# Kernel tuning notes

Measured on AMD Instinct MI355X. Metric: run time of the kernel, lower is better.

The kernel has to match this reference:

```python
import jax, jax.numpy as jnp
import numpy as np

LAT = 4; K = 4; NP = 3 * K - 1; HID = 16; NT = 10; BOUND = 5.0
_in_deg = np.arange(1, LAT + 1)
_hd = (np.arange(HID) % (LAT - 1)) + 1
M1 = jnp.asarray((_hd[:, None] >= _in_deg[None, :]).astype(np.float32))  # [HID, LAT]
M2 = jnp.asarray((_hd[:, None] >= _hd[None, :]).astype(np.float32))      # [HID, HID]
M3 = jnp.asarray((np.repeat(_in_deg, NP)[:, None] > _hd[None, :]).astype(np.float32))  # [LAT*NP, HID]


def _subm(x, m, w, b):
    # submanifold conv: inactive inputs are zero, output restricted to active sites
    y = jax.lax.conv_general_dilated(x, w, (1, 1), 'SAME', dimension_numbers=('NHWC', 'HWIO', 'NHWC')) + b
    return jnp.where(m[..., None], y, 0.0)


def _maxpool(x, m, kh, kw):
    neg = jnp.asarray(-1e30, x.dtype)
    xm = jnp.where(m[..., None], x, neg)
    y = jax.lax.reduce_window(xm, neg, jax.lax.max, (1, kh, kw, 1), (1, kh, kw, 1), 'VALID')
    mo = jax.lax.reduce_window(m.astype(x.dtype), 0.0, jax.lax.max, (1, kh, kw), (1, kh, kw), 'VALID') > 0
    return jnp.where(mo[..., None], y, 0.0), mo


def _invconv(x, w, b, mo):
    # sparse inverse conv with kernel == stride of paired pool: non-overlapping transposed conv
    kh, kw, ci, co = w.shape
    B, h, wd, _ = x.shape
    y = jnp.einsum('bhwc,ijcd->bhiwjd', x, w).reshape(B, h * kh, wd * kw, co) + b
    return jnp.where(mo[..., None], y, 0.0)


def _rqs(x, uw, uh, ud):
    # monotonic rational-quadratic spline, identity outside [-BOUND, BOUND]
    shp = x.shape
    widths = jax.nn.softmax(uw, -1) * (2 * BOUND)
    heights = jax.nn.softmax(uh, -1) * (2 * BOUND)
    edge = jnp.full(shp + (1,), -BOUND, x.dtype)
    xk = jnp.concatenate([edge, jnp.cumsum(widths, -1) - BOUND], -1)
    yk = jnp.concatenate([edge, jnp.cumsum(heights, -1) - BOUND], -1)
    one = jnp.ones(shp + (1,), x.dtype)
    dk = jnp.concatenate([one, jax.nn.softplus(ud), one], -1)
    inside = (x >= -BOUND) & (x <= BOUND)
    xc = jnp.clip(x, -BOUND, BOUND)
    idx = jnp.clip(jnp.sum((xc[..., None] >= xk[..., :-1]).astype(jnp.int32), -1) - 1, 0, K - 1)[..., None]
    g = lambda a, i: jnp.take_along_axis(a, i, -1)[..., 0]
    x0, x1 = g(xk, idx), g(xk, idx + 1)
    y0, y1 = g(yk, idx), g(yk, idx + 1)
    d0, d1 = g(dk, idx), g(dk, idx + 1)
    dx = x1 - x0
    dy = y1 - y0
    s = dy / dx
    t = (xc - x0) / dx
    den = s + (d1 + d0 - 2 * s) * t * (1 - t)
    y = y0 + dy * (s * t * t + d0 * t * (1 - t)) / den
    ld = jnp.log(s * s * (d1 * t * t + 2 * s * t * (1 - t) + d0 * (1 - t) ** 2)) - 2 * jnp.log(den)
    return jnp.where(inside, y, x), jnp.where(inside, ld, 0.0)


def _nsf(z, fW1, fb1, fW2, fb2, fW3, fb3):
    ld_tot = jnp.zeros(z.shape[:-1], z.dtype)
    for t in range(NT):
        h = jax.nn.relu(z @ (fW1[t] * M1).T + fb1[t])
        h = jax.nn.relu(h @ (fW2[t] * M2).T + fb2[t])
        p = (h @ (fW3[t] * M3).T + fb3[t]).reshape(z.shape[:-1] + (LAT, NP))
        z, ld = _rqs(z, p[..., :K], p[..., K:2 * K], p[..., 2 * K:])
        ld_tot = ld_tot + ld.sum(-1)
        if t < NT - 1:
            z = z[..., ::-1]
    return z, ld_tot


def _forward(x, eps, w1, b1, w2, b2, w3, b3, wmu, bmu, wlv, blv, wlin, blin, u1, bu1, w4, b4, u2, bu2, w5, b5, u3, bu3, w6, b6, fW1, fb1, fW2, fb2, fW3, fb3):
    xn = jnp.transpose(x, (0, 2, 3, 1))  # NCHW -> NHWC
    m0 = jnp.any(xn != 0, axis=-1)       # active sites (spconv from_dense)
    lrelu = lambda v: jax.nn.leaky_relu(v, 0.01)
    y = lrelu(_subm(xn, m0, w1, b1))
    y, m1 = _maxpool(y, m0, 2, 2)
    y = lrelu(_subm(y, m1, w2, b2))
    y, m2 = _maxpool(y, m1, 5, 2)
    y = lrelu(_subm(y, m2, w3, b3))
    y, m3 = _maxpool(y, m2, 5, 2)        # [B, 4, 16, 32]
    mu = jnp.where(m3[..., None], y @ wmu.T + bmu, 0.0)
    logvar = jnp.where(m3[..., None], y @ wlv.T + blv, 0.0)
    std = jnp.exp(0.5 * logvar)
    z0 = mu + eps * std
    z, log_det = _nsf(z0, fW1, fb1, fW2, fb2, fW3, fb3)
    LOG2PI = 1.8378770664093453
    log_q0 = jnp.sum(-0.5 * ((z0 - mu) / std) ** 2 - jnp.log(std) - 0.5 * LOG2PI, -1)
    log_p = jnp.sum(-0.5 * z * z - 0.5 * LOG2PI, -1)
    kld_pc = log_q0 - log_det - log_p
    kld = jnp.sum(jnp.where(m3, kld_pc, 0.0), axis=(1, 2))  # index_add over batch indices
    zf = jnp.where(m3[..., None], z, 0.0)
    dec = jnp.where(m3[..., None], zf @ wlin.T + blin, 0.0)
    y = _invconv(dec, u1, bu1, m2)
    y = _subm(y, m2, w4, b4)
    y = _invconv(y, u2, bu2, m1)
    y = _subm(y, m1, w5, b5)
    y = _invconv(y, u3, bu3, m0)
    y = _subm(y, m0, w6, b6)
    out = jnp.transpose(y, (0, 3, 1, 2))  # back to NCHW like .dense()
    return out, mu, logvar, kld, zf


def setup_inputs():
    key = jax.random.key(0)
    ks = iter(jax.random.split(key, 80))
    B, C, H, W = 128, 6, 200, 128
    d = {}
    x = jax.random.normal(next(ks), (B, C, H, W), jnp.float32)
    keep = jax.random.uniform(next(ks), (B, 1, H, W)) < 0.15
    d['x'] = jnp.where(keep, x, 0.0)
    d['eps'] = jax.random.normal(next(ks), (B, 4, 16, LAT), jnp.float32)
    def p(name, shape, s=0.1):
        d[name] = jax.random.normal(next(ks), shape, jnp.float32) * s
    p('w1', (3, 3, 6, 8)); p('b1', (8,))
    p('w2', (3, 3, 8, 16)); p('b2', (16,))
    p('w3', (3, 3, 16, 32)); p('b3', (32,))
    p('wmu', (LAT, 32)); p('bmu', (LAT,))
    p('wlv', (LAT, 32)); p('blv', (LAT,))
    p('wlin', (32, LAT)); p('blin', (32,))
    p('u1', (5, 2, 32, 32)); p('bu1', (32,))
    p('w4', (3, 3, 32, 16)); p('b4', (16,))
    p('u2', (5, 2, 16, 16)); p('bu2', (16,))
    p('w5', (3, 3, 16, 8)); p('b5', (8,))
    p('u3', (2, 2, 8, 8)); p('bu3', (8,))
    p('w6', (3, 3, 8, 6)); p('b6', (6,))
    p('fW1', (NT, HID, LAT)); p('fb1', (NT, HID))
    p('fW2', (NT, HID, HID)); p('fb2', (NT, HID))
    p('fW3', (NT, LAT * NP, HID)); p('fb3', (NT, LAT * NP))
    return d


def reference(x, eps, w1, b1, w2, b2, w3, b3, wmu, bmu, wlv, blv, wlin, blin, u1, bu1, w4, b4, u2, bu2, w5, b5, u3, bu3, w6, b6, fW1, fb1, fW2, fb2, fW3, fb3):
    return _forward(x, eps, w1, b1, w2, b2, w3, b3, wmu, bmu, wlv, blv, wlin, blin, u1, bu1, w4, b4, u2, bu2, w5, b5, u3, bu3, w6, b6, fW1, fb1, fW2, fb2, fW3, fb3)
```

## Files before the change

### kernel.cpp

```cpp
#include <hip/hip_runtime.h>
#include <math.h>

constexpr int NB=128;
constexpr int NH0=200, NW0=128, NC0=6;
constexpr int NH1=100, NW1=64,  NC1=8;
constexpr int NH2=20,  NW2=32,  NC2=16;
constexpr int NH3=4,   NW3=16,  NC3=32;
constexpr int LAT=4, NPp=11, HID=16, NT=10;
constexpr float BOUNDf=5.0f;
constexpr float LOG2PI=1.8378770664093453f;

__device__ __forceinline__ float fexpf(float v){ return __expf(v); }
__device__ __forceinline__ float flogf(float v){ return __logf(v); }
__device__ __forceinline__ float softplusf(float v){ return v>20.f ? v : __logf(1.f+__expf(v)); }
__device__ __forceinline__ float lrelu(float v){ return v>0.f ? v : 0.01f*v; }

__global__ __launch_bounds__(256) void k_conv1pool(
    const float* __restrict__ x, const float* __restrict__ w1, const float* __restrict__ b1,
    float* __restrict__ y1p, unsigned char* __restrict__ m0, unsigned char* __restrict__ m1){
  __shared__ float xs[6][18][24];
  __shared__ float ws1[54][8];
  __shared__ float b1s[8];
  int blk = blockIdx.x;
  int b  = blk / 104;
  int t  = blk % 104;
  int th = t >> 3, tw = t & 7;
  int h0 = th*16, w0 = tw*16;
  int tid = threadIdx.x;
  for (int i=tid;i<432;i+=256) ws1[i>>3][i&7] = w1[i];
  if (tid<8) b1s[tid]=b1[tid];
  for (int i=tid;i<6*18*18;i+=256){
    int ci=i/324; int rem=i-ci*324; int r=rem/18, c=rem-r*18;
    int h=h0-1+r, w=w0-1+c;
    float v=0.f;
    if (h>=0 && h<NH0 && w>=0 && w<NW0) v = x[((size_t)(b*NC0+ci)*NH0+h)*NW0+w];
    xs[ci][r][c]=v;
  }
  __syncthreads();
  int r = tid>>4, c = tid&15;
  int h = h0+r, w = w0+c;
  bool inb = (h < NH0);
  float c0v=xs[0][r+1][c+1], c1v=xs[1][r+1][c+1], c2v=xs[2][r+1][c+1];
  float c3v=xs[3][r+1][c+1], c4v=xs[4][r+1][c+1], c5v=xs[5][r+1][c+1];
  bool act = inb && ((c0v!=0.f)||(c1v!=0.f)||(c2v!=0.f)||(c3v!=0.f)||(c4v!=0.f)||(c5v!=0.f));
  if (inb) m0[(b*NH0+h)*NW0+w] = act?1:0;
  float a[8];
  #pragma unroll
  for (int co=0;co<8;co++) a[co]=b1s[co];
  #pragma unroll 1
  for (int kh=0;kh<3;kh++)
  #pragma unroll 1
  for (int kw=0;kw<3;kw++){
    #pragma unroll
    for (int ci=0;ci<6;ci++){
      float v = xs[ci][r+kh][c+kw];
      const float* wv = ws1[(kh*3+kw)*6+ci];
      #pragma unroll
      for (int co=0;co<8;co++) a[co]=fmaf(v,wv[co],a[co]);
    }
  }
  #pragma unroll
  for (int co=0;co<8;co++) a[co] = act ? lrelu(a[co]) : -1e30f;
  float best[8];
  #pragma unroll
  for (int co=0;co<8;co++){
    float v = a[co];
    v = fmaxf(v, __shfl_xor(v,1));
    v = fmaxf(v, __shfl_xor(v,16));
    best[co]=v;
  }
  float af = act?1.f:0.f;
  af = fmaxf(af, __shfl_xor(af,1));
  af = fmaxf(af, __shfl_xor(af,16));
  bool anyact = af>0.f;
  bool rep = ((r&1)==0) && ((c&1)==0);
  if (rep && inb){
    int hp=h>>1, wp=w>>1;
    float4 o0,o1;
    if (anyact){
      o0=make_float4(best[0],best[1],best[2],best[3]);
      o1=make_float4(best[4],best[5],best[6],best[7]);
    } else { o0=make_float4(0,0,0,0); o1=o0; }
    float4* yp = (float4*)(y1p + (((size_t)b*NH1+hp)*NW1+wp)*8);
    yp[0]=o0; yp[1]=o1;
    m1[(b*NH1+hp)*NW1+wp] = anyact?1:0;
  }
}

__global__ __launch_bounds__(256) void k_conv2pool(
    const float* __restrict__ yin, const unsigned char* __restrict__ m1,
    const float* __restrict__ w2, const float* __restrict__ b2,
    float* __restrict__ yout, unsigned char* __restrict__ m2){
  __shared__ float ys[8][27][35];
  __shared__ unsigned char msl[27][35];
  __shared__ float w2s[72][16];
  __shared__ float b2s[16];
  int blk = blockIdx.x;
  int b  = blk >> 3;
  int t  = blk & 7;
  int th = t >> 1, tw = t & 1;
  int r0 = th*25 - 1, c0 = tw*32 - 1;
  int tid = threadIdx.x;
  for (int i=tid;i<1152;i+=256) w2s[i>>4][i&15] = w2[i];
  if (tid<16) b2s[tid]=b2[tid];
  for (int p=tid;p<27*34;p+=256){
    int r=p/34, c=p-(p/34)*34;
    int h1=r0+r, w1c=c0+c;
    bool ok = (h1>=0 && h1<NH1 && w1c>=0 && w1c<NW1);
    msl[r][c] = ok ? m1[(b*NH1+h1)*NW1+w1c] : 0;
    float4 v0=make_float4(0,0,0,0), v1=v0;
    if (ok){
      const float4* pp = (const float4*)(yin + (((size_t)b*NH1+h1)*NW1+w1c)*8);
      v0=pp[0]; v1=pp[1];
    }
    ys[0][r][c]=v0.x; ys[1][r][c]=v0.y; ys[2][r][c]=v0.z; ys[3][r][c]=v0.w;
    ys[4][r][c]=v1.x; ys[5][r][c]=v1.y; ys[6][r][c]=v1.z; ys[7][r][c]=v1.w;
  }
  __syncthreads();
  if (tid < 160){
    int oid = tid >> 1, coq = tid & 1;
    int co0 = coq*8;
    int lh = oid >> 4, lw = oid & 15;
    int h2 = th*5+lh, w2c = tw*16+lw;
    float best[8];
    #pragma unroll
    for (int co=0;co<8;co++) best[co]=-1e30f;
    bool many=false;
    #pragma unroll 1
    for (int i=0;i<5;i++)
    #pragma unroll 1
    for (int j=0;j<2;j++){
      int r = lh*5+i+1, c = lw*2+j+1;
      if (!msl[r][c]) continue;
      many=true;
      float a[8];
      #pragma unroll
      for (int co=0;co<8;co++) a[co]=b2s[co0+co];
      #pragma unroll 1
      for (int kh=0;kh<3;kh++)
      #pragma unroll 1
      for (int kw=0;kw<3;kw++){
        #pragma unroll
        for (int ci=0;ci<8;ci++){
          float v = ys[ci][r-1+kh][c-1+kw];
          const float* wr = w2s[(kh*3+kw)*8+ci];
          #pragma unroll
          for (int co=0;co<8;co++) a[co]=fmaf(v,wr[co0+co],a[co]);
        }
      }
      #pragma unroll
      for (int co=0;co<8;co++) best[co]=fmaxf(best[co], lrelu(a[co]));
    }
    float4 o0,o1;
    if (many){
      o0=make_float4(best[0],best[1],best[2],best[3]);
      o1=make_float4(best[4],best[5],best[6],best[7]);
    } else { o0=make_float4(0,0,0,0); o1=o0; }
    float4* op = (float4*)(yout + (((size_t)b*NH2+h2)*NW2+w2c)*16 + co0);
    op[0]=o0; op[1]=o1;
    if (coq==0) m2[(b*NH2+h2)*NW2+w2c] = many?1:0;
  }
}

__global__ __launch_bounds__(256) void k_conv3pool(
    const float* __restrict__ yin, const unsigned char* __restrict__ m2,
    const float* __restrict__ w3, const float* __restrict__ b3,
    float* __restrict__ yout, unsigned char* __restrict__ m3,
    float* __restrict__ out_kld){
  __shared__ float ys[16][20][33];
  __shared__ unsigned char msl[20][32];
  __shared__ float w3s[144][32];
  __shared__ float b3s[32];
  int b = blockIdx.x;
  int tid = threadIdx.x;
  if (tid==0) out_kld[b]=0.f;
  for (int i=tid;i<4608;i+=256) w3s[i>>5][i&31] = w3[i];
  if (tid<32) b3s[tid]=b3[tid];
  for (int p=tid;p<640;p+=256){
    int r=p>>5, c=p&31;
    msl[r][c] = m2[(b*NH2+r)*NW2+c];
    const float4* pp = (const float4*)(yin + (((size_t)b*NH2+r)*NW2+c)*16);
    float4 q0=pp[0],q1=pp[1],q2=pp[2],q3=pp[3];
    ys[0][r][c]=q0.x; ys[1][r][c]=q0.y; ys[2][r][c]=q0.z; ys[3][r][c]=q0.w;
    ys[4][r][c]=q1.x; ys[5][r][c]=q1.y; ys[6][r][c]=q1.z; ys[7][r][c]=q1.w;
    ys[8][r][c]=q2.x; ys[9][r][c]=q2.y; ys[10][r][c]=q2.z; ys[11][r][c]=q2.w;
    ys[12][r][c]=q3.x; ys[13][r][c]=q3.y; ys[14][r][c]=q3.z; ys[15][r][c]=q3.w;
  }
  __syncthreads();
  int p = tid>>2, coq = tid&3;
  int co0 = coq*8;
  int hp = p>>4, wp = p&15;
  float best[8];
  #pragma unroll
  for (int co=0;co<8;co++) best[co]=-1e30f;
  bool many=false;
  #pragma unroll 1
  for (int i=0;i<5;i++)
  #pragma unroll 1
  for (int j=0;j<2;j++){
    int h2 = hp*5+i, w2c = wp*2+j;
    if (!msl[h2][w2c]) continue;
    many=true;
    float a[8];
    #pragma unroll
    for (int co=0;co<8;co++) a[co]=b3s[co0+co];
    #pragma unroll 1
    for (int kh=0;kh<3;kh++){
      int hh=h2+kh-1;
      if (hh<0||hh>=NH2) continue;
      #pragma unroll 1
      for (int kw=0;kw<3;kw++){
        int ww=w2c+kw-1;
        if (ww<0||ww>=NW2) continue;
        #pragma unroll
        for (int ci=0;ci<16;ci++){
          float v = ys[ci][hh][ww];
          const float* wr = w3s[(kh*3+kw)*16+ci];
          #pragma unroll
          for (int co=0;co<8;co++) a[co]=fmaf(v,wr[co0+co],a[co]);
        }
      }
    }
    #pragma unroll
    for (int co=0;co<8;co++) best[co]=fmaxf(best[co], lrelu(a[co]));
  }
  float4 o0,o1;
  if (many){
    o0=make_float4(best[0],best[1],best[2],best[3]);
    o1=make_float4(best[4],best[5],best[6],best[7]);
  } else { o0=make_float4(0,0,0,0); o1=o0; }
  float4* op = (float4*)(yout + ((size_t)(b*64+p))*32 + co0);
  op[0]=o0; op[1]=o1;
  if (coq==0) m3[b*64+p] = many?1:0;
}

__global__ __launch_bounds__(64) void k_latent(
    const float* __restrict__ y3p, const unsigned char* __restrict__ m3,
    const float* __restrict__ eps,
    const float* __restrict__ wmu, const float* __restrict__ bmu,
    const float* __restrict__ wlv, const float* __restrict__ blv,
    const float* __restrict__ wlin, const float* __restrict__ blin,
    const float* __restrict__ fW1, const float* __restrict__ fb1,
    const float* __restrict__ fW2, const float* __restrict__ fb2,
    const float* __restrict__ fW3, const float* __restrict__ fb3,
    float* __restrict__ out_mu, float* __restrict__ out_lv,
    float* __restrict__ out_kld, float* __restrict__ out_zf,
    float* __restrict__ dec)
{
  __shared__ __align__(16) float sW1[NT*HID*LAT];
  __shared__ float sb1[NT*HID];
  __shared__ __align__(16) float sW2[NT*HID*HID];
  __shared__ float sb2[NT*HID];
  __shared__ __align__(16) float sW3[NT*LAT*NPp*HID];
  __shared__ float sb3[NT*LAT*NPp];
  __shared__ __align__(16) float swmu[LAT*NC3];
  __shared__ __align__(16) float swlv[LAT*NC3];
  __shared__ __align__(16) float slin[NC3*LAT];
  __shared__ float sbmu[LAT], sblv[LAT], sblin[NC3];
  int tid = threadIdx.x;
  for (int i=tid;i<NT*HID*LAT;i+=64){ int j=i&3; int r=(i>>2)%HID; sW1[i]=fW1[i]*(((r%3+1)>=(j+1))?1.f:0.f); }
  for (int i=tid;i<NT*HID;i+=64){ sb1[i]=fb1[i]; sb2[i]=fb2[i]; }
  for (int i=tid;i<NT*HID*HID;i+=64){ int j=i&15; int r=(i>>4)%HID; sW2[i]=fW2[i]*(((r%3+1)>=(j%3+1))?1.f:0.f); }
  for (int i=tid;i<NT*LAT*NPp*HID;i+=64){ int j=i&15; int r=(i>>4)%(LAT*NPp); sW3[i]=fW3[i]*(((r/NPp+1)>(j%3+1))?1.f:0.f); }
  for (int i=tid;i<NT*LAT*NPp;i+=64) sb3[i]=fb3[i];
  for (int i=tid;i<LAT*NC3;i+=64){ swmu[i]=wmu[i]; swlv[i]=wlv[i]; slin[i]=wlin[i]; }
  if (tid<LAT){ sbmu[tid]=bmu[tid]; sblv[tid]=blv[tid]; }
  for (int i=tid;i<NC3;i+=64) sblin[i]=blin[i];
  __syncthreads();

  int blk = blockIdx.x;
  int b   = blk >> 2;
  int gpos = b*64 + (blk&3)*16 + (tid>>2);
  int g = tid & 3;
  bool msk = m3[gpos]!=0;
  float kld_part = 0.f;
  if (msk){
    const float4* yp = (const float4*)(y3p + (size_t)gpos*NC3);
    const float4* wm = (const float4*)(swmu + g*NC3);
    const float4* wl = (const float4*)(swlv + g*NC3);
    float mu_g = sbmu[g], lv_g = sblv[g];
    #pragma unroll
    for (int q=0;q<8;q++){
      float4 yq = yp[q], a = wm[q], c = wl[q];
      mu_g = fmaf(yq.x,a.x, fmaf(yq.y,a.y, fmaf(yq.z,a.z, fmaf(yq.w,a.w, mu_g))));
      lv_g = fmaf(yq.x,c.x, fmaf(yq.y,c.y, fmaf(yq.z,c.z, fmaf(yq.w,c.w, lv_g))));
    }
    float std_g = fexpf(0.5f*lv_g);
    float ev_g  = eps[(size_t)gpos*LAT+g];
    float z0_g  = fmaf(ev_g, std_g, mu_g);
    float zg = z0_g;
    float z[4];
    z[g]=zg; z[g^1]=__shfl_xor(zg,1); z[g^2]=__shfl_xor(zg,2); z[g^3]=__shfl_xor(zg,3);
    float ld_g = 0.f;
    for (int t=0;t<NT;t++){
      float h1[16];
      const float4* W1t = (const float4*)(sW1 + t*HID*LAT);
      const float*  b1t = sb1 + t*HID;
      #pragma unroll
      for (int i2=0;i2<16;i2++){
        float4 w = W1t[i2];
        float a = b1t[i2];
        a = fmaf(z[0],w.x, fmaf(z[1],w.y, fmaf(z[2],w.z, fmaf(z[3],w.w, a))));
        h1[i2]=fmaxf(a,0.f);
      }
      float h2o[4];
      const float* W2t = sW2 + t*HID*HID;
      const float* b2t = sb2 + t*HID;
      #pragma unroll
      for (int k=0;k<4;k++){
        int row = g*4+k;
        const float4* wr = (const float4*)(W2t + row*HID);
        float a = b2t[row];
        #pragma unroll
        for (int q=0;q<4;q++){
          float4 w = wr[q];
          a = fmaf(h1[q*4+0],w.x, fmaf(h1[q*4+1],w.y, fmaf(h1[q*4+2],w.z, fmaf(h1[q*4+3],w.w, a))));
        }
        h2o[k]=fmaxf(a,0.f);
      }
      float h2[16];
      #pragma unroll
      for (int k=0;k<4;k++) h2[g*4+k]=h2o[k];
      #pragma unroll
      for (int mski=1;mski<4;mski++){
        int og = g^mski;
        #pragma unroll
        for (int k=0;k<4;k++) h2[og*4+k]=__shfl_xor(h2o[k],mski);
      }
      float p[NPp];
      const float* W3t = sW3 + t*LAT*NPp*HID;
      const float* b3t = sb3 + t*LAT*NPp;
      #pragma unroll
      for (int r=0;r<NPp;r++){
        int row = g*NPp+r;
        const float4* wr = (const float4*)(W3t + row*HID);
        float a = b3t[row];
        #pragma unroll
        for (int q=0;q<4;q++){
          float4 w = wr[q];
          a = fmaf(h2[q*4+0],w.x, fmaf(h2[q*4+1],w.y, fmaf(h2[q*4+2],w.z, fmaf(h2[q*4+3],w.w, a))));
        }
        p[r]=a;
      }
      float mw=fmaxf(fmaxf(p[0],p[1]),fmaxf(p[2],p[3]));
      float e0=fexpf(p[0]-mw), e1=fexpf(p[1]-mw), e2=fexpf(p[2]-mw), e3=fexpf(p[3]-mw);
      float wsc=10.f/(e0+e1+e2+e3);
      float xk1=fmaf(e0,wsc,-BOUNDf), xk2=fmaf(e1,wsc,xk1), xk3=fmaf(e2,wsc,xk2), xk4=fmaf(e3,wsc,xk3);
      float mh=fmaxf(fmaxf(p[4],p[5]),fmaxf(p[6],p[7]));
      float f0=fexpf(p[4]-mh), f1=fexpf(p[5]-mh), f2=fexpf(p[6]-mh), f3=fexpf(p[7]-mh);
      float hsc=10.f/(f0+f1+f2+f3);
      float yk1=fmaf(f0,hsc,-BOUNDf), yk2=fmaf(f1,hsc,yk1), yk3=fmaf(f2,hsc,yk2), yk4=fmaf(f3,hsc,yk3);
      float dk1=softplusf(p[8]), dk2=softplusf(p[9]), dk3=softplusf(p[10]);
      float xv=z[g];
      bool inside = (xv>=-BOUNDf)&&(xv<=BOUNDf);
      float xc=fminf(fmaxf(xv,-BOUNDf),BOUNDf);
      float x0=-BOUNDf, x1=xk1, y0=-BOUNDf, y1=yk1, d0=1.f, d1=dk1;
      if (xc>=xk1){x0=xk1;x1=xk2;y0=yk1;y1=yk2;d0=dk1;d1=dk2;}
      if (xc>=xk2){x0=xk2;x1=xk3;y0=yk2;y1=yk3;d0=dk2;d1=dk3;}
      if (xc>=xk3){x0=xk3;x1=xk4;y0=yk3;y1=yk4;d0=dk3;d1=1.f;}
      float dxv=x1-x0, dyv=y1-y0;
      float sl=dyv/dxv, ttv=(xc-x0)/dxv, omt=1.f-ttv;
      float den=sl + (d1+d0-2.f*sl)*ttv*omt;
      float yo=y0 + dyv*(sl*ttv*ttv + d0*ttv*omt)/den;
      float ldv=flogf(sl*sl*(d1*ttv*ttv + 2.f*sl*ttv*omt + d0*omt*omt)) - 2.f*flogf(den);
      float zn_g = inside ? yo : xv;
      ld_g += inside ? ldv : 0.f;
      float znf[4];
      znf[g]=zn_g; znf[g^1]=__shfl_xor(zn_g,1); znf[g^2]=__shfl_xor(zn_g,2); znf[g^3]=__shfl_xor(zn_g,3);
      if (t<NT-1){ z[0]=znf[3]; z[1]=znf[2]; z[2]=znf[1]; z[3]=znf[0]; }
      else       { z[0]=znf[0]; z[1]=znf[1]; z[2]=znf[2]; z[3]=znf[3]; }
    }
    float lq_g = -0.5f*ev_g*ev_g - 0.5f*lv_g - 0.5f*LOG2PI;
    float lp_g = -0.5f*z[g]*z[g] - 0.5f*LOG2PI;
    kld_part = lq_g - ld_g - lp_g;
    out_mu[(size_t)gpos*LAT+g]=mu_g;
    out_lv[(size_t)gpos*LAT+g]=lv_g;
    out_zf[(size_t)gpos*LAT+g]=z[g];
    float4 d0v, d1v;
    {
      float dv[8];
      #pragma unroll
      for (int k=0;k<8;k++){
        int c = g*8+k;
        const float4 w = ((const float4*)slin)[c];
        dv[k] = fmaf(z[0],w.x, fmaf(z[1],w.y, fmaf(z[2],w.z, fmaf(z[3],w.w, sblin[c]))));
      }
      d0v=make_float4(dv[0],dv[1],dv[2],dv[3]);
      d1v=make_float4(dv[4],dv[5],dv[6],dv[7]);
    }
    float4* dp = (float4*)(dec + (size_t)gpos*NC3 + g*8);
    dp[0]=d0v; dp[1]=d1v;
  } else {
    out_mu[(size_t)gpos*LAT+g]=0.f;
    out_lv[(size_t)gpos*LAT+g]=0.f;
    out_zf[(size_t)gpos*LAT+g]=0.f;
    float4 zv = make_float4(0,0,0,0);
    float4* dp = (float4*)(dec + (size_t)gpos*NC3 + g*8);
    dp[0]=zv; dp[1]=zv;
  }
  float s = kld_part;
  s += __shfl_xor(s,1);  s += __shfl_xor(s,2);
  s += __shfl_xor(s,4);  s += __shfl_xor(s,8);
  s += __shfl_xor(s,16); s += __shfl_xor(s,32);
  if (tid==0) atomicAdd(&out_kld[b], s);
}

__global__ __launch_bounds__(256) void k_ic4(
    const float* __restrict__ dec, const unsigned char* __restrict__ m2,
    const float* __restrict__ u1, const float* __restrict__ bu1,
    const float* __restrict__ w4, const float* __restrict__ b4,
    float* __restrict__ t2){
  __shared__ __align__(16) float vs[12][18][32];
  __shared__ __align__(16) float w4s[288][16];
  __shared__ unsigned char msl[12][18];
  int blk = blockIdx.x;
  int b  = blk >> 2;
  int t  = blk & 3;
  int th = t >> 1, tw = t & 1;
  int h0 = th*10, w0 = tw*16;
  int tid = threadIdx.x;
  for (int i=tid;i<288*16;i+=256) w4s[i>>4][i&15] = w4[i];
  if (tid < 216){
    int lr = tid/18, lc = tid%18;
    int h2 = h0-1+lr, w2 = w0-1+lc;
    bool mk = (h2>=0 && h2<NH2 && w2>=0 && w2<NW2) && m2[(b*NH2+h2)*NW2+w2];
    msl[lr][lc] = mk?1:0;
    float acc[32];
    if (mk){
      const float* dp = dec + (((size_t)b*NH3 + h2/5)*NW3 + w2/2)*NC3;
      const float* up = u1 + ((h2%5)*2 + (w2&1))*1024;
      #pragma unroll
      for (int co=0;co<32;co++) acc[co]=bu1[co];
      #pragma unroll 1
      for (int ci=0;ci<32;ci++){
        float dv = dp[ci];
        const float* ur = up + ci*32;
        #pragma unroll
        for (int co=0;co<32;co++) acc[co]=fmaf(dv,ur[co],acc[co]);
      }
    } else {
      #pragma unroll
      for (int co=0;co<32;co++) acc[co]=0.f;
    }
    #pragma unroll
    for (int co=0;co<32;co++) vs[lr][lc][co]=acc[co];
  }
  __syncthreads();
  if (tid < 160){
    int lh = tid/16, lw = tid%16;
    int h2 = h0+lh, w2 = w0+lw;
    float a[16];
    if (msl[lh+1][lw+1]){
      #pragma unroll
      for (int co=0;co<16;co++) a[co]=b4[co];
      #pragma unroll 1
      for (int kh=0;kh<3;kh++)
      #pragma unroll 1
      for (int kw=0;kw<3;kw++){
        const float* vp = vs[lh+kh][lw+kw];
        #pragma unroll
        for (int ci=0;ci<32;ci++){
          float v = vp[ci];
          const float* wr = w4s[(kh*3+kw)*32+ci];
          #pragma unroll
          for (int co=0;co<16;co++) a[co]=fmaf(v,wr[co],a[co]);
        }
      }
    } else {
      #pragma unroll
      for (int co=0;co<16;co++) a[co]=0.f;
    }
    float* op = t2 + (((size_t)b*NH2+h2)*NW2+w2)*NC2;
    #pragma unroll
    for (int co=0;co<16;co++) op[co]=a[co];
  }
}

__global__ __launch_bounds__(256) void k_ic5(
    const float* __restrict__ t2, const unsigned char* __restrict__ m1,
    const float* __restrict__ u2, const float* __restrict__ bu2,
    const float* __restrict__ w5, const float* __restrict__ b5,
    float* __restrict__ t4){
  __shared__ __align__(16) float vs[12][18][16];
  __shared__ __align__(16) float w5s[144][8];
  __shared__ unsigned char msl[12][18];
  int blk = blockIdx.x;
  int b  = blk / 40;
  int t  = blk % 40;
  int th = t >> 2, tw = t & 3;
  int h0 = th*10, w0 = tw*16;
  int tid = threadIdx.x;
  for (int i=tid;i<144*8;i+=256) w5s[i>>3][i&7] = w5[i];
  if (tid < 216){
    int lr = tid/18, lc = tid%18;
    int h1 = h0-1+lr, w1c = w0-1+lc;
    bool mk = (h1>=0 && h1<NH1 && w1c>=0 && w1c<NW1) && m1[(b*NH1+h1)*NW1+w1c];
    msl[lr][lc] = mk?1:0;
    float acc[16];
    if (mk){
      const float* dp = t2 + (((size_t)b*NH2 + h1/5)*NW2 + w1c/2)*NC2;
      const float* up = u2 + ((h1%5)*2 + (w1c&1))*256;
      #pragma unroll
      for (int co=0;co<16;co++) acc[co]=bu2[co];
      #pragma unroll 1
      for (int ci=0;ci<16;ci++){
        float dv = dp[ci];
        const float* ur = up + ci*16;
        #pragma unroll
        for (int co=0;co<16;co++) acc[co]=fmaf(dv,ur[co],acc[co]);
      }
    } else {
      #pragma unroll
      for (int co=0;co<16;co++) acc[co]=0.f;
    }
    #pragma unroll
    for (int co=0;co<16;co++) vs[lr][lc][co]=acc[co];
  }
  __syncthreads();
  if (tid < 160){
    int lh = tid/16, lw = tid%16;
    int h1 = h0+lh, w1c = w0+lw;
    float a[8];
    if (msl[lh+1][lw+1]){
      #pragma unroll
      for (int co=0;co<8;co++) a[co]=b5[co];
      #pragma unroll 1
      for (int kh=0;kh<3;kh++)
      #pragma unroll 1
      for (int kw=0;kw<3;kw++){
        const float* vp = vs[lh+kh][lw+kw];
        #pragma unroll
        for (int ci=0;ci<16;ci++){
          float v = vp[ci];
          const float* wr = w5s[(kh*3+kw)*16+ci];
          #pragma unroll
          for (int co=0;co<8;co++) a[co]=fmaf(v,wr[co],a[co]);
        }
      }
    } else {
      #pragma unroll
      for (int co=0;co<8;co++) a[co]=0.f;
    }
    float* op = t4 + (((size_t)b*NH1+h1)*NW1+w1c)*NC1;
    #pragma unroll
    for (int co=0;co<8;co++) op[co]=a[co];
  }
}

__global__ __launch_bounds__(256) void k_inv3conv6(
    const float* __restrict__ t4, const unsigned char* __restrict__ m0,
    const float* __restrict__ u3, const float* __restrict__ bu3,
    const float* __restrict__ w6, const float* __restrict__ b6,
    float* __restrict__ out){
  __shared__ float vs[8][18][68];
  __shared__ unsigned char msl[18][66];
  __shared__ float u3s[4][8][8];
  __shared__ float w6s[9][8][6];
  __shared__ float bu3s[8];
  __shared__ float b6s[6];
  int blk = blockIdx.x;
  int b  = blk / 26;
  int t  = blk % 26;
  int th = t >> 1, tw = t & 1;
  int h0 = th*16, w0 = tw*64;
  int tid = threadIdx.x;
  for (int i=tid;i<256;i+=256){ u3s[i>>6][(i>>3)&7][i&7]=u3[i]; }
  for (int i=tid;i<432;i+=256){ int tap=i/48; int rem=i%48; w6s[tap][rem/6][rem%6]=w6[i]; }
  if (tid<8) bu3s[tid]=bu3[tid];
  if (tid<6) b6s[tid]=b6[tid];
  __syncthreads();
  for (int p=tid;p<18*66;p+=256){
    int r=p/66, c=p-(p/66)*66;
    int h=h0-1+r, w=w0-1+c;
    bool act = (h>=0 && h<NH0 && w>=0 && w<NW0) && m0[(b*NH0+h)*NW0+w];
    msl[r][c] = act?1:0;
    float v8[8];
    if (act){
      const float4* tp = (const float4*)(t4 + (((size_t)b*NH1 + (h>>1))*NW1 + (w>>1))*8);
      float4 q0=tp[0], q1=tp[1];
      float tin[8]={q0.x,q0.y,q0.z,q0.w,q1.x,q1.y,q1.z,q1.w};
      const float (*up)[8] = u3s[(h&1)*2+(w&1)];
      #pragma unroll
      for (int c8=0;c8<8;c8++) v8[c8]=bu3s[c8];
      #pragma unroll
      for (int ci=0;ci<8;ci++){
        float v=tin[ci];
        #pragma unroll
        for (int c8=0;c8<8;c8++) v8[c8]=fmaf(v, up[ci][c8], v8[c8]);
      }
    } else {
      #pragma unroll
      for (int c8=0;c8<8;c8++) v8[c8]=0.f;
    }
    #pragma unroll
    for (int c8=0;c8<8;c8++) vs[c8][r][c]=v8[c8];
  }
  __syncthreads();
  #pragma unroll 1
  for (int k=0;k<4;k++){
    int p = tid + k*256;
    int lh = p>>6, lw = p&63;
    int h = h0+lh, w = w0+lw;
    if (h >= NH0) continue;
    float acc[6];
    if (msl[lh+1][lw+1]){
      #pragma unroll
      for (int co=0;co<6;co++) acc[co]=b6s[co];
      #pragma unroll 1
      for (int kh=0;kh<3;kh++)
      #pragma unroll 1
      for (int kw=0;kw<3;kw++){
        const float (*wt)[6] = w6s[kh*3+kw];
        #pragma unroll
        for (int ci=0;ci<8;ci++){
          float v = vs[ci][lh+kh][lw+kw];
          #pragma unroll
          for (int co=0;co<6;co++) acc[co]=fmaf(v, wt[ci][co], acc[co]);
        }
      }
    } else {
      #pragma unroll
      for (int co=0;co<6;co++) acc[co]=0.f;
    }
    size_t base = (size_t)b*6*NH0*NW0 + (size_t)h*NW0 + w;
    #pragma unroll
    for (int co=0;co<6;co++) out[base + (size_t)co*NH0*NW0] = acc[co];
  }
}

extern "C" void kernel_launch(void* const* d_in, const int* in_sizes, int n_in,
                              void* d_out, int out_size, void* d_ws, size_t ws_size,
                              hipStream_t stream){
  (void)in_sizes; (void)n_in; (void)out_size; (void)ws_size;
  const float* x    = (const float*)d_in[0];
  const float* eps  = (const float*)d_in[1];
  const float* w1   = (const float*)d_in[2];
  const float* b1   = (const float*)d_in[3];
  const float* w2   = (const float*)d_in[4];
  const float* b2   = (const float*)d_in[5];
  const float* w3   = (const float*)d_in[6];
  const float* b3   = (const float*)d_in[7];
  const float* wmu  = (const float*)d_in[8];
  const float* bmu  = (const float*)d_in[9];
  const float* wlv  = (const float*)d_in[10];
  const float* blv  = (const float*)d_in[11];
  const float* wlin = (const float*)d_in[12];
  const float* blin = (const float*)d_in[13];
  const float* u1   = (const float*)d_in[14];
  const float* bu1  = (const float*)d_in[15];
  const float* w4   = (const float*)d_in[16];
  const float* b4   = (const float*)d_in[17];
  const float* u2   = (const float*)d_in[18];
  const float* bu2  = (const float*)d_in[19];
  const float* w5   = (const float*)d_in[20];
  const float* b5   = (const float*)d_in[21];
  const float* u3   = (const float*)d_in[22];
  const float* bu3  = (const float*)d_in[23];
  const float* w6   = (const float*)d_in[24];
  const float* b6   = (const float*)d_in[25];
  const float* fW1  = (const float*)d_in[26];
  const float* fb1  = (const float*)d_in[27];
  const float* fW2  = (const float*)d_in[28];
  const float* fb2  = (const float*)d_in[29];
  const float* fW3  = (const float*)d_in[30];
  const float* fb3  = (const float*)d_in[31];

  char* ws = (char*)d_ws;
  unsigned char* m0 = (unsigned char*)(ws);
  unsigned char* m1 = (unsigned char*)(ws + 3276800);
  unsigned char* m2 = (unsigned char*)(ws + 4096000);
  unsigned char* m3 = (unsigned char*)(ws + 4177920);
  float* y1p = (float*)(ws + 4194304);
  float* y2p = (float*)(ws + 30408704);
  float* y3p = (float*)(ws + 35651584);
  float* dec = (float*)(ws + 36700160);
  float* t2  = y2p;
  float* t4  = y1p;

  float* out   = (float*)d_out;
  float* o_mu  = out + 19660800;
  float* o_lv  = out + 19693568;
  float* o_kld = out + 19726336;
  float* o_zf  = out + 19726464;

  k_conv1pool<<<13312,256,0,stream>>>(x, w1, b1, y1p, m0, m1);
  k_conv2pool<<< 1024,256,0,stream>>>(y1p, m1, w2, b2, y2p, m2);
  k_conv3pool<<<  128,256,0,stream>>>(y2p, m2, w3, b3, y3p, m3, o_kld);
  k_latent   <<<  512, 64,0,stream>>>(y3p, m3, eps, wmu,bmu,wlv,blv,wlin,blin,
                                      fW1,fb1,fW2,fb2,fW3,fb3, o_mu,o_lv,o_kld,o_zf, dec);
  k_ic4      <<<  512,256,0,stream>>>(dec, m2, u1, bu1, w4, b4, t2);
  k_ic5      <<< 5120,256,0,stream>>>(t2, m1, u2, bu2, w5, b5, t4);
  k_inv3conv6<<< 3328,256,0,stream>>>(t4, m0, u3, bu3, w6, b6, out);
}
```

Measured before the change: 449.5 us.

## Compute two vertically adjacent outputs per thread in conv1 with taller tiles

The first conv+pool kernel now gives each thread two vertically adjacent output pixels, using 32x16 tiles instead of 16x16. The vertical half of the 2x2 max-pool happens in registers, so one shuffle level disappears, and every weight read from shared memory feeds two FMAs. The inner loops are fully unrolled and the block count drops. The cost is more registers per thread and extra halo rows in the last tile, which is partly out of bounds because 200 is not a multiple of 32.

```diff
diff --git a/kernel.cpp b/kernel.cpp
--- a/kernel.cpp
+++ b/kernel.cpp
@@ -18,64 +18,75 @@
 __global__ __launch_bounds__(256) void k_conv1pool(
     const float* __restrict__ x, const float* __restrict__ w1, const float* __restrict__ b1,
     float* __restrict__ y1p, unsigned char* __restrict__ m0, unsigned char* __restrict__ m1){
-  __shared__ float xs[6][18][24];
+  __shared__ float xs[6][34][19];
   __shared__ float ws1[54][8];
   __shared__ float b1s[8];
   int blk = blockIdx.x;
-  int b  = blk / 104;
-  int t  = blk % 104;
+  int b  = blk / 56;
+  int t  = blk % 56;
   int th = t >> 3, tw = t & 7;
-  int h0 = th*16, w0 = tw*16;
+  int h0 = th*32, w0 = tw*16;
   int tid = threadIdx.x;
   for (int i=tid;i<432;i+=256) ws1[i>>3][i&7] = w1[i];
   if (tid<8) b1s[tid]=b1[tid];
-  for (int i=tid;i<6*18*18;i+=256){
-    int ci=i/324; int rem=i-ci*324; int r=rem/18, c=rem-r*18;
+  for (int i=tid;i<6*34*18;i+=256){
+    int ci=i/612; int rem=i-ci*612; int r=rem/18, c=rem-r*18;
     int h=h0-1+r, w=w0-1+c;
     float v=0.f;
     if (h>=0 && h<NH0 && w>=0 && w<NW0) v = x[((size_t)(b*NC0+ci)*NH0+h)*NW0+w];
     xs[ci][r][c]=v;
   }
   __syncthreads();
-  int r = tid>>4, c = tid&15;
-  int h = h0+r, w = w0+c;
-  bool inb = (h < NH0);
-  float c0v=xs[0][r+1][c+1], c1v=xs[1][r+1][c+1], c2v=xs[2][r+1][c+1];
-  float c3v=xs[3][r+1][c+1], c4v=xs[4][r+1][c+1], c5v=xs[5][r+1][c+1];
-  bool act = inb && ((c0v!=0.f)||(c1v!=0.f)||(c2v!=0.f)||(c3v!=0.f)||(c4v!=0.f)||(c5v!=0.f));
-  if (inb) m0[(b*NH0+h)*NW0+w] = act?1:0;
-  float a[8];
+  int pp = tid>>4, pj = tid&15;
+  int hA = h0 + 2*pp;
+  int w  = w0 + pj;
+  bool inbA = (hA   < NH0);
+  bool inbB = (hA+1 < NH0);
+  bool actA=false, actB=false;
   #pragma unroll
-  for (int co=0;co<8;co++) a[co]=b1s[co];
-  #pragma unroll 1
-  for (int kh=0;kh<3;kh++)
-  #pragma unroll 1
-  for (int kw=0;kw<3;kw++){
-    #pragma unroll
-    for (int ci=0;ci<6;ci++){
-      float v = xs[ci][r+kh][c+kw];
-      const float* wv = ws1[(kh*3+kw)*6+ci];
-      #pragma unroll
-      for (int co=0;co<8;co++) a[co]=fmaf(v,wv[co],a[co]);
-    }
-  }
+  for (int ci=0;ci<6;ci++){
+    actA |= (xs[ci][2*pp+1][pj+1]!=0.f);
+    actB |= (xs[ci][2*pp+2][pj+1]!=0.f);
+  }
+  actA = actA && inbA;
+  actB = actB && inbB;
+  if (inbA) m0[(b*NH0+hA  )*NW0+w] = actA?1:0;
+  if (inbB) m0[(b*NH0+hA+1)*NW0+w] = actB?1:0;
+  float aA[8], aB[8];
   #pragma unroll
-  for (int co=0;co<8;co++) a[co] = act ? lrelu(a[co]) : -1e30f;
+  for (int co=0;co<8;co++){ aA[co]=b1s[co]; aB[co]=b1s[co]; }
+  #pragma unroll
+  for (int ci=0;ci<6;ci++){
+    #pragma unroll
+    for (int kh=0;kh<3;kh++){
+      #pragma unroll
+      for (int kw=0;kw<3;kw++){
+        float vA = xs[ci][2*pp+kh  ][pj+kw];
+        float vB = xs[ci][2*pp+kh+1][pj+kw];
+        const float* wv = ws1[(kh*3+kw)*6+ci];
+        #pragma unroll
+        for (int co=0;co<8;co++){
+          float wc = wv[co];
+          aA[co]=fmaf(vA,wc,aA[co]);
+          aB[co]=fmaf(vB,wc,aB[co]);
+        }
+      }
+    }
+  }
   float best[8];
   #pragma unroll
   for (int co=0;co<8;co++){
-    float v = a[co];
-    v = fmaxf(v, __shfl_xor(v,1));
-    v = fmaxf(v, __shfl_xor(v,16));
-    best[co]=v;
-  }
-  float af = act?1.f:0.f;
+    float va = actA ? lrelu(aA[co]) : -1e30f;
+    float vb = actB ? lrelu(aB[co]) : -1e30f;
+    float v  = fmaxf(va,vb);
+    best[co] = fmaxf(v, __shfl_xor(v,1));
+  }
+  float af = (actA||actB) ? 1.f : 0.f;
   af = fmaxf(af, __shfl_xor(af,1));
-  af = fmaxf(af, __shfl_xor(af,16));
   bool anyact = af>0.f;
-  bool rep = ((r&1)==0) && ((c&1)==0);
-  if (rep && inb){
-    int hp=h>>1, wp=w>>1;
+  int hp = th*16 + pp;
+  if (((pj&1)==0) && hp < NH1){
+    int wp = tw*8 + (pj>>1);
     float4 o0,o1;
     if (anyact){
       o0=make_float4(best[0],best[1],best[2],best[3]);
@@ -683,7 +694,7 @@
   float* o_kld = out + 19726336;
   float* o_zf  = out + 19726464;
 
-  k_conv1pool<<<13312,256,0,stream>>>(x, w1, b1, y1p, m0, m1);
+  k_conv1pool<<< 7168,256,0,stream>>>(x, w1, b1, y1p, m0, m1);
   k_conv2pool<<< 1024,256,0,stream>>>(y1p, m1, w2, b2, y2p, m2);
   k_conv3pool<<<  128,256,0,stream>>>(y2p, m2, w3, b3, y3p, m3, o_kld);
   k_latent   <<<  512, 64,0,stream>>>(y3p, m3, eps, wmu,bmu,wlv,blv,wlin,blin,
```

Measured after the change: 440.5 us. -2.0%, faster.

## Compute 2x2 pooled quad per thread in conv1 with 32x32 tiles

Applied to the files above, without the earlier changes.

The first conv+pool kernel now gives each thread the 2x2 pre-pool output quad that feeds one pooled cell, using a 32x32 input tile per block instead of 16x16. The max-pool is done in registers instead of with cross-lane shuffles, and all threads write outputs rather than one in four. Window loads are reused across neighbouring pixels, weights are read as float4, and the two mask bytes per row are written as one 16-bit store. In exchange the kernel uses more registers for the accumulators and more shared memory, launches fewer blocks, and does partly wasted work on the last row of tiles, where 200 rows do not divide evenly by 32.

```diff
diff --git a/kernel.cpp b/kernel.cpp
--- a/kernel.cpp
+++ b/kernel.cpp
@@ -18,64 +18,86 @@
 __global__ __launch_bounds__(256) void k_conv1pool(
     const float* __restrict__ x, const float* __restrict__ w1, const float* __restrict__ b1,
     float* __restrict__ y1p, unsigned char* __restrict__ m0, unsigned char* __restrict__ m1){
-  __shared__ float xs[6][18][24];
+  __shared__ float xs[6][34][35];
   __shared__ float ws1[54][8];
   __shared__ float b1s[8];
   int blk = blockIdx.x;
-  int b  = blk / 104;
-  int t  = blk % 104;
-  int th = t >> 3, tw = t & 7;
-  int h0 = th*16, w0 = tw*16;
+  int b  = blk / 28;
+  int t  = blk % 28;
+  int th = t >> 2, tw = t & 3;
+  int h0 = th*32, w0 = tw*32;
   int tid = threadIdx.x;
   for (int i=tid;i<432;i+=256) ws1[i>>3][i&7] = w1[i];
   if (tid<8) b1s[tid]=b1[tid];
-  for (int i=tid;i<6*18*18;i+=256){
-    int ci=i/324; int rem=i-ci*324; int r=rem/18, c=rem-r*18;
-    int h=h0-1+r, w=w0-1+c;
+  for (int i=tid;i<6*34*34;i+=256){
+    int ci=i/1156; int rem=i-ci*1156; int r2=rem/34, c2=rem-r2*34;
+    int h=h0-1+r2, w=w0-1+c2;
     float v=0.f;
     if (h>=0 && h<NH0 && w>=0 && w<NW0) v = x[((size_t)(b*NC0+ci)*NH0+h)*NW0+w];
-    xs[ci][r][c]=v;
+    xs[ci][r2][c2]=v;
   }
   __syncthreads();
   int r = tid>>4, c = tid&15;
-  int h = h0+r, w = w0+c;
-  bool inb = (h < NH0);
-  float c0v=xs[0][r+1][c+1], c1v=xs[1][r+1][c+1], c2v=xs[2][r+1][c+1];
-  float c3v=xs[3][r+1][c+1], c4v=xs[4][r+1][c+1], c5v=xs[5][r+1][c+1];
-  bool act = inb && ((c0v!=0.f)||(c1v!=0.f)||(c2v!=0.f)||(c3v!=0.f)||(c4v!=0.f)||(c5v!=0.f));
-  if (inb) m0[(b*NH0+h)*NW0+w] = act?1:0;
-  float a[8];
+  bool a00=false,a01=false,a10=false,a11=false;
   #pragma unroll
-  for (int co=0;co<8;co++) a[co]=b1s[co];
+  for (int ci=0;ci<6;ci++){
+    a00 |= (xs[ci][2*r+1][2*c+1]!=0.f);
+    a01 |= (xs[ci][2*r+1][2*c+2]!=0.f);
+    a10 |= (xs[ci][2*r+2][2*c+1]!=0.f);
+    a11 |= (xs[ci][2*r+2][2*c+2]!=0.f);
+  }
+  float acc[4][8];
+  #pragma unroll
+  for (int px=0;px<4;px++)
+    #pragma unroll
+    for (int co=0;co<8;co++) acc[px][co]=b1s[co];
   #pragma unroll 1
-  for (int kh=0;kh<3;kh++)
-  #pragma unroll 1
-  for (int kw=0;kw<3;kw++){
-    #pragma unroll
-    for (int ci=0;ci<6;ci++){
-      float v = xs[ci][r+kh][c+kw];
-      const float* wv = ws1[(kh*3+kw)*6+ci];
-      #pragma unroll
-      for (int co=0;co<8;co++) a[co]=fmaf(v,wv[co],a[co]);
-    }
-  }
-  #pragma unroll
-  for (int co=0;co<8;co++) a[co] = act ? lrelu(a[co]) : -1e30f;
+  for (int ci=0;ci<6;ci++){
+    #pragma unroll 1
+    for (int kh=0;kh<3;kh++){
+      const float* xr0 = &xs[ci][2*r+kh][2*c];
+      const float* xr1 = &xs[ci][2*r+kh+1][2*c];
+      float t0a=xr0[0], t0b=xr0[1], t0c=xr0[2], t0d=xr0[3];
+      float t1a=xr1[0], t1b=xr1[1], t1c=xr1[2], t1d=xr1[3];
+      const float4* wrow = (const float4*)&ws1[(kh*3)*6+ci][0];
+      #pragma unroll
+      for (int kw=0;kw<3;kw++){
+        float4 wlo = wrow[kw*12], whi = wrow[kw*12+1];
+        float wv[8] = {wlo.x,wlo.y,wlo.z,wlo.w,whi.x,whi.y,whi.z,whi.w};
+        float t00 = (kw==0)?t0a:((kw==1)?t0b:t0c);
+        float t01 = (kw==0)?t0b:((kw==1)?t0c:t0d);
+        float t10 = (kw==0)?t1a:((kw==1)?t1b:t1c);
+        float t11 = (kw==0)?t1b:((kw==1)?t1c:t1d);
+        #pragma unroll
+        for (int co=0;co<8;co++){
+          float wc = wv[co];
+          acc[0][co]=fmaf(t00,wc,acc[0][co]);
+          acc[1][co]=fmaf(t01,wc,acc[1][co]);
+          acc[2][co]=fmaf(t10,wc,acc[2][co]);
+          acc[3][co]=fmaf(t11,wc,acc[3][co]);
+        }
+      }
+    }
+  }
+  int hA = h0 + 2*r;
+  bool valid = (hA < NH0);
+  bool anyact = (a00|a01|a10|a11) && valid;
   float best[8];
   #pragma unroll
   for (int co=0;co<8;co++){
-    float v = a[co];
-    v = fmaxf(v, __shfl_xor(v,1));
-    v = fmaxf(v, __shfl_xor(v,16));
-    best[co]=v;
-  }
-  float af = act?1.f:0.f;
-  af = fmaxf(af, __shfl_xor(af,1));
-  af = fmaxf(af, __shfl_xor(af,16));
-  bool anyact = af>0.f;
-  bool rep = ((r&1)==0) && ((c&1)==0);
-  if (rep && inb){
-    int hp=h>>1, wp=w>>1;
+    float v0 = a00 ? lrelu(acc[0][co]) : -1e30f;
+    float v1 = a01 ? lrelu(acc[1][co]) : -1e30f;
+    float v2 = a10 ? lrelu(acc[2][co]) : -1e30f;
+    float v3 = a11 ? lrelu(acc[3][co]) : -1e30f;
+    best[co] = fmaxf(fmaxf(v0,v1),fmaxf(v2,v3));
+  }
+  if (valid){
+    int wA = w0 + 2*c;
+    unsigned short p0 = (unsigned short)((a00?1:0) | ((a01?1:0)<<8));
+    unsigned short p1 = (unsigned short)((a10?1:0) | ((a11?1:0)<<8));
+    *(unsigned short*)(m0 + (size_t)(b*NH0+hA  )*NW0 + wA) = p0;
+    *(unsigned short*)(m0 + (size_t)(b*NH0+hA+1)*NW0 + wA) = p1;
+    int hp = th*16 + r, wp = tw*16 + c;
     float4 o0,o1;
     if (anyact){
       o0=make_float4(best[0],best[1],best[2],best[3]);
@@ -683,7 +705,7 @@
   float* o_kld = out + 19726336;
   float* o_zf  = out + 19726464;
 
-  k_conv1pool<<<13312,256,0,stream>>>(x, w1, b1, y1p, m0, m1);
+  k_conv1pool<<< 3584,256,0,stream>>>(x, w1, b1, y1p, m0, m1);
   k_conv2pool<<< 1024,256,0,stream>>>(y1p, m1, w2, b2, y2p, m2);
   k_conv3pool<<<  128,256,0,stream>>>(y2p, m2, w3, b3, y3p, m3, o_kld);
   k_latent   <<<  512, 64,0,stream>>>(y3p, m3, eps, wmu,bmu,wlv,blv,wlin,blin,
```

Result: faster. 437.1 us (-2.8%).
